# Kernel tuning notes

Hardware: AMD Instinct MI355X
Metric: run time of the kernel (lower is better)

Reference implementation:

```python
import jax, jax.numpy as jnp
import numpy as np

N, D, R, E = 10000, 1024, 8, 80000


def setup_inputs() -> dict:
    key = jax.random.key(0)
    ks = jax.random.split(key, 8)
    s = 1.0 / np.sqrt(D)
    x = jax.random.normal(ks[0], (N, D), dtype=jnp.float32)
    edge_index = jax.random.randint(ks[1], (2, E), 0, N, dtype=jnp.int64)
    edge_type = jax.random.randint(ks[2], (E,), 0, R, dtype=jnp.int64)
    weight = jax.random.normal(ks[3], (R, D, D), dtype=jnp.float32) * s  # per-relation W_r
    root = jax.random.normal(ks[4], (D, D), dtype=jnp.float32) * s      # root/self-loop weight
    bias = jnp.zeros((D,), dtype=jnp.float32)
    w_gate = jax.random.normal(ks[5], (2 * D, D), dtype=jnp.float32) * (1.0 / np.sqrt(2 * D))
    b_gate = jnp.zeros((D,), dtype=jnp.float32)
    return {"x": x, "edge_index": edge_index, "edge_type": edge_type,
            "weight": weight, "root": root, "bias": bias,
            "w_gate": w_gate, "b_gate": b_gate}


def _rgcn(x, edge_index, edge_type, weight, root, bias):
    # PyG RGCNConv (aggr='mean'): per relation r, mean-aggregate x[src] into dst,
    # then transform by W_r (aggregate-then-transform, equivalent by linearity).
    src, dst = edge_index[0], edge_index[1]
    msgs = x[src]                                   # [E, D] gather
    out = x @ root + bias                           # root/self connection
    n = x.shape[0]
    for r in range(weight.shape[0]):                # small fixed relation loop
        mask = (edge_type == r).astype(x.dtype)     # [E]
        sums = jax.ops.segment_sum(msgs * mask[:, None], dst, num_segments=n)
        cnt = jax.ops.segment_sum(mask, dst, num_segments=n)
        mean = sums / jnp.maximum(cnt, 1.0)[:, None]
        out = out + mean @ weight[r]
    return out


def reference(x, edge_index, edge_type, weight, root, bias, w_gate, b_gate):
    u = _rgcn(x, edge_index, edge_type, weight, root, bias)
    # dropout p=0 -> identity
    z = jnp.concatenate([u, x], axis=1) @ w_gate + b_gate
    h = jnp.tanh(u) * z + x * (1.0 - z)
    return h
```

## Files before the change

kernel.cpp:

```cpp
#include <hip/hip_runtime.h>
#include <math.h>

typedef unsigned short u16;
typedef __attribute__((ext_vector_type(8))) short bf16x8;
typedef __attribute__((ext_vector_type(4))) float f32x4;

static constexpr int kN = 10000;
static constexpr int kNpad = 10240;
static constexpr int kD = 1024;
static constexpr int kR = 8;
static constexpr int kE = 80000;
static constexpr int kKz = 2 * kD;
static constexpr int kCrows = kNpad * (kR + 1);
static constexpr int kTilesY1 = kCrows / 128;

#define GLB(p) ((const __attribute__((address_space(1))) unsigned int*)(const void*)(p))
#define LDSP(p) ((__attribute__((address_space(3))) unsigned int*)(p))

__device__ __forceinline__ u16 f2bf(float f) {
    union { float f; unsigned int i; } c; c.f = f;
    unsigned int u = c.i;
    return (u16)((u + 0x7FFFu + ((u >> 16) & 1u)) >> 16);
}
__device__ __forceinline__ float bf2f(u16 u) {
    union { unsigned int i; float f; } c; c.i = ((unsigned int)u) << 16;
    return c.f;
}
__device__ __forceinline__ ushort4 f2bf4(float4 v) {
    ushort4 o; o.x = f2bf(v.x); o.y = f2bf(v.y); o.z = f2bf(v.z); o.w = f2bf(v.w);
    return o;
}

__global__ void zero16(uint4* __restrict__ p, long n16) {
    long i = (long)blockIdx.x * blockDim.x + threadIdx.x;
    long st = (long)gridDim.x * blockDim.x;
    uint4 z = make_uint4(0, 0, 0, 0);
    for (; i < n16; i += st) p[i] = z;
}

__global__ void mark_edges(const int* __restrict__ src, const int* __restrict__ dst,
                           const int* __restrict__ etype,
                           int* __restrict__ cntd, int* __restrict__ flag) {
    int e = blockIdx.x * blockDim.x + threadIdx.x;
    if (e < kE) {
        atomicAdd(&cntd[dst[e]], 1);
        flag[etype[e] * kN + src[e]] = 1;
    }
}

__global__ __launch_bounds__(1024) void scan_rowptr(const int* __restrict__ cnt,
                                                    int* __restrict__ rowptr,
                                                    int* __restrict__ cursor) {
    __shared__ int wsum[16];
    __shared__ int carry;
    const int tid = threadIdx.x;
    const int lane = tid & 63;
    const int w = tid >> 6;
    if (tid == 0) carry = 0;
    const int nchunk = (kN + 1024) / 1024;
    for (int ch = 0; ch < nchunk; ++ch) {
        int idx = ch * 1024 + tid;
        int v = (idx < kN) ? cnt[idx] : 0;
        int s = v;
#pragma unroll
        for (int off = 1; off < 64; off <<= 1) {
            int t = __shfl_up(s, off, 64);
            if (lane >= off) s += t;
        }
        if (lane == 63) wsum[w] = s;
        __syncthreads();
        if (w == 0 && lane < 16) {
            int t = wsum[lane];
#pragma unroll
            for (int off = 1; off < 16; off <<= 1) {
                int tt = __shfl_up(t, off, 64);
                if (lane >= off) t += tt;
            }
            wsum[lane] = t;
        }
        __syncthreads();
        int wpre = (w > 0) ? wsum[w - 1] : 0;
        int incl = s + wpre + carry;
        int excl = incl - v;
        if (idx <= kN) rowptr[idx] = excl;
        if (idx < kN) cursor[idx] = 0;
        __syncthreads();
        if (tid == 1023) carry = incl;
        __syncthreads();
    }
}

__global__ __launch_bounds__(1024) void compact_scan(const int* __restrict__ flag,
                                                     int* __restrict__ row_src,
                                                     int* __restrict__ pos_tab,
                                                     int* __restrict__ relcnt9) {
    const int tid = threadIdx.x;
    if (blockIdx.x == kR) {
        for (int i = tid; i < kNpad; i += 1024) row_src[i] = i;
        if (tid == 0) relcnt9[0] = kN;
        return;
    }
    const int r = blockIdx.x;
    const int base = kNpad * (r + 1);
    __shared__ int wsum[16];
    __shared__ int carry;
    const int lane = tid & 63;
    const int w = tid >> 6;
    if (tid == 0) carry = 0;
    const int nchunk = (kN + 1023) / 1024;
    for (int ch = 0; ch < nchunk; ++ch) {
        int idx = ch * 1024 + tid;
        int v = (idx < kN) ? flag[r * kN + idx] : 0;
        int s = v;
#pragma unroll
        for (int off = 1; off < 64; off <<= 1) {
            int t = __shfl_up(s, off, 64);
            if (lane >= off) s += t;
        }
        if (lane == 63) wsum[w] = s;
        __syncthreads();
        if (w == 0 && lane < 16) {
            int t = wsum[lane];
#pragma unroll
            for (int off = 1; off < 16; off <<= 1) {
                int tt = __shfl_up(t, off, 64);
                if (lane >= off) t += tt;
            }
            wsum[lane] = t;
        }
        __syncthreads();
        int wpre = (w > 0) ? wsum[w - 1] : 0;
        int incl = s + wpre + carry;
        int excl = incl - v;
        if (idx < kN && v) {
            row_src[base + excl] = idx;
            pos_tab[r * kN + idx] = base + excl;
        }
        __syncthreads();
        if (tid == 1023) carry = incl;
        __syncthreads();
    }
    if (tid == 0) relcnt9[r + 1] = carry;
}

__global__ void fill_edges(const int* __restrict__ src, const int* __restrict__ dst,
                           const int* __restrict__ etype, const int* __restrict__ rowptr,
                           int* __restrict__ cursor, const int* __restrict__ pos_tab,
                           int* __restrict__ erec) {
    int e = blockIdx.x * blockDim.x + threadIdx.x;
    if (e < kE) {
        int d = dst[e], r = etype[e], s = src[e];
        int pos = rowptr[d] + atomicAdd(&cursor[d], 1);
        erec[pos] = (pos_tab[r * kN + s] << 3) | r;
    }
}

__global__ void cvt_x(const float* __restrict__ x, u16* __restrict__ ga) {
    int row = blockIdx.x;
    int c = threadIdx.x << 2;
    float4 v = *reinterpret_cast<const float4*>(x + (size_t)row * kD + c);
    *reinterpret_cast<ushort4*>(ga + (size_t)row * kKz + kD + c) = f2bf4(v);
}

__global__ void transpose_to_bf16(const float* __restrict__ S, u16* __restrict__ D,
                                  int rows, int cols, int ldD) {
    S += (size_t)blockIdx.z * rows * cols;
    D += (size_t)blockIdx.z * rows * cols;
    __shared__ float t[32][33];
    int c0 = blockIdx.x * 32, r0 = blockIdx.y * 32;
    int x = threadIdx.x, y = threadIdx.y;
#pragma unroll
    for (int i = 0; i < 32; i += 8)
        t[y + i][x] = S[(size_t)(r0 + y + i) * cols + c0 + x];
    __syncthreads();
#pragma unroll
    for (int i = 0; i < 32; i += 8)
        D[(size_t)(c0 + y + i) * ldD + r0 + x] = f2bf(t[x][y + i]);
}

__global__ __launch_bounds__(256) void aggregate(const u16* __restrict__ yc,
                                                 const float* __restrict__ bias,
                                                 const int* __restrict__ rowptr,
                                                 const int* __restrict__ erec,
                                                 u16* __restrict__ ga) {
    const int d = blockIdx.x;
    const int c = threadIdx.x << 2;
    const int e0 = rowptr[d], e1 = rowptr[d + 1];

    __shared__ float rs[kR];
    if (threadIdx.x == 0) {
        int cc[kR] = {0, 0, 0, 0, 0, 0, 0, 0};
        for (int e = e0; e < e1; ++e) cc[erec[e] & 7]++;
#pragma unroll
        for (int r = 0; r < kR; ++r) rs[r] = 1.0f / fmaxf((float)cc[r], 1.0f);
    }
    __syncthreads();

    ushort4 rv = *reinterpret_cast<const ushort4*>(yc + (size_t)d * kD + c);
    float4 bv = *reinterpret_cast<const float4*>(bias + c);
    float4 acc = make_float4(bf2f(rv.x) + bv.x, bf2f(rv.y) + bv.y,
                             bf2f(rv.z) + bv.z, bf2f(rv.w) + bv.w);

    int e = e0;
    for (; e + 3 < e1; e += 4) {
        int rec0 = erec[e], rec1 = erec[e + 1], rec2 = erec[e + 2], rec3 = erec[e + 3];
        ushort4 v0 = *reinterpret_cast<const ushort4*>(yc + (size_t)(rec0 >> 3) * kD + c);
        ushort4 v1 = *reinterpret_cast<const ushort4*>(yc + (size_t)(rec1 >> 3) * kD + c);
        ushort4 v2 = *reinterpret_cast<const ushort4*>(yc + (size_t)(rec2 >> 3) * kD + c);
        ushort4 v3 = *reinterpret_cast<const ushort4*>(yc + (size_t)(rec3 >> 3) * kD + c);
        float s0 = rs[rec0 & 7], s1 = rs[rec1 & 7], s2 = rs[rec2 & 7], s3 = rs[rec3 & 7];
        acc.x += s0 * bf2f(v0.x); acc.y += s0 * bf2f(v0.y);
        acc.z += s0 * bf2f(v0.z); acc.w += s0 * bf2f(v0.w);
        acc.x += s1 * bf2f(v1.x); acc.y += s1 * bf2f(v1.y);
        acc.z += s1 * bf2f(v1.z); acc.w += s1 * bf2f(v1.w);
        acc.x += s2 * bf2f(v2.x); acc.y += s2 * bf2f(v2.y);
        acc.z += s2 * bf2f(v2.z); acc.w += s2 * bf2f(v2.w);
        acc.x += s3 * bf2f(v3.x); acc.y += s3 * bf2f(v3.y);
        acc.z += s3 * bf2f(v3.z); acc.w += s3 * bf2f(v3.w);
    }
    for (; e < e1; ++e) {
        int rec = erec[e];
        float sc = rs[rec & 7];
        ushort4 v = *reinterpret_cast<const ushort4*>(yc + (size_t)(rec >> 3) * kD + c);
        acc.x += sc * bf2f(v.x); acc.y += sc * bf2f(v.y);
        acc.z += sc * bf2f(v.z); acc.w += sc * bf2f(v.w);
    }
    *reinterpret_cast<ushort4*>(ga + (size_t)d * kKz + c) = f2bf4(acc);
}

__global__ __launch_bounds__(256, 3) void gemm_compact(
    const u16* __restrict__ xb, int ldx,
    const u16* __restrict__ Bt9,
    const int* __restrict__ row_src, const int* __restrict__ relcnt9,
    u16* __restrict__ yc)
{
    const int t0 = blockIdx.y;
    const int relidx = t0 / 80;
    const int lt = t0 - relidx * 80;
    if (lt * 128 >= relcnt9[relidx]) return;

    __shared__ u16 sA[3][128 * 32];
    __shared__ u16 sB[3][128 * 32];

    const int tid = threadIdx.x;
    const int wave = tid >> 6;
    const int lane = tid & 63;

    const int row0 = t0 * 128;
    const int col0 = blockIdx.x * 128;

    const int srow = wave * 16 + (lane >> 2);
    const int scol = (((lane & 3) ^ ((srow >> 1) & 3)) * 8);

    const u16* gA0 = xb + (size_t)row_src[row0 + srow] * ldx + scol;
    const u16* gA1 = xb + (size_t)row_src[row0 + 64 + srow] * ldx + scol;
    const u16* gB0 = Bt9 + (size_t)(relidx * kD + col0 + srow) * kD + scol;
    const u16* gB1 = Bt9 + (size_t)(relidx * kD + col0 + 64 + srow) * kD + scol;

    const int lof0 = (wave * 16) * 32;
    const int lof1 = (64 + wave * 16) * 32;

    const int mq = (wave >> 1) * 64;
    const int nq = (wave & 1) * 64;
    const int fm = lane & 15;
    const int fkx = (((lane >> 4) ^ ((fm >> 1) & 3))) * 8;

    f32x4 zf = {0.0f, 0.0f, 0.0f, 0.0f};
    f32x4 acc[4][4];
#pragma unroll
    for (int i = 0; i < 4; ++i)
#pragma unroll
        for (int j = 0; j < 4; ++j) acc[i][j] = zf;

    auto stage = [&](int s) {
        __builtin_amdgcn_global_load_lds(GLB(gA0), LDSP(sA[s] + lof0), 16, 0, 0);
        __builtin_amdgcn_global_load_lds(GLB(gA1), LDSP(sA[s] + lof1), 16, 0, 0);
        __builtin_amdgcn_global_load_lds(GLB(gB0), LDSP(sB[s] + lof0), 16, 0, 0);
        __builtin_amdgcn_global_load_lds(GLB(gB1), LDSP(sB[s] + lof1), 16, 0, 0);
        gA0 += 32; gA1 += 32; gB0 += 32; gB1 += 32;
    };

    constexpr int T = kD / 32;
    stage(0);
    stage(1);

    int s = 0;
    for (int t = 0; t < T; ++t) {
        if (t + 2 < T) {
            stage(s == 0 ? 2 : (s - 1));
            asm volatile("s_waitcnt vmcnt(8)" ::: "memory");
        } else if (t + 1 < T) {
            asm volatile("s_waitcnt vmcnt(4)" ::: "memory");
        } else {
            asm volatile("s_waitcnt vmcnt(0)" ::: "memory");
        }
        __builtin_amdgcn_s_barrier();
        asm volatile("" ::: "memory");

        const u16* cA = sA[s];
        const u16* cB = sB[s];
        bf16x8 af[4], bfr[4];
#pragma unroll
        for (int i = 0; i < 4; ++i)
            af[i] = *reinterpret_cast<const bf16x8*>(&cA[(mq + i * 16 + fm) * 32 + fkx]);
#pragma unroll
        for (int j = 0; j < 4; ++j)
            bfr[j] = *reinterpret_cast<const bf16x8*>(&cB[(nq + j * 16 + fm) * 32 + fkx]);
#pragma unroll
        for (int i = 0; i < 4; ++i)
#pragma unroll
            for (int j = 0; j < 4; ++j)
                acc[i][j] = __builtin_amdgcn_mfma_f32_16x16x32_bf16(bfr[j], af[i], acc[i][j], 0, 0, 0);

        asm volatile("" ::: "memory");
        __builtin_amdgcn_s_barrier();
        s = (s == 2) ? 0 : (s + 1);
    }

    const int cq = (lane >> 4) * 4;
#pragma unroll
    for (int i = 0; i < 4; ++i) {
        int row = row0 + mq + i * 16 + fm;
#pragma unroll
        for (int j = 0; j < 4; ++j) {
            int col = col0 + nq + j * 16 + cq;
            f32x4 v = acc[i][j];
            ushort4 o;
            o.x = f2bf(v[0]); o.y = f2bf(v[1]); o.z = f2bf(v[2]); o.w = f2bf(v[3]);
            *reinterpret_cast<ushort4*>(yc + (size_t)row * kD + col) = o;
        }
    }
}

__global__ __launch_bounds__(256, 3) void gemm_mfma_gate(
    const u16* __restrict__ A, int lda,
    const u16* __restrict__ Bt, int ldb, int K,
    int M, const float* __restrict__ bias,
    float* __restrict__ Cf, const u16* __restrict__ uga, const float* __restrict__ xo)
{
    __shared__ u16 sA[3][128 * 32];
    __shared__ u16 sB[3][128 * 32];

    const int tid = threadIdx.x;
    const int wave = tid >> 6;
    const int lane = tid & 63;

    constexpr int GX = kD / 128;
    constexpr int GY = kNpad / 128;
    const int lin = blockIdx.y * GX + blockIdx.x;
    const int xcd = lin & 7;
    const int pos = lin >> 3;
    const int ty = xcd * (GY / 8) + (pos >> 3);
    const int tx = pos & 7;

    const int row0 = ty * 128;
    const int col0 = tx * 128;

    const int srow = wave * 16 + (lane >> 2);
    const int scol = (((lane & 3) ^ ((srow >> 1) & 3)) * 8);

    const u16* gA0 = A + (size_t)(row0 + srow) * lda + scol;
    const u16* gA1 = A + (size_t)(row0 + 64 + srow) * lda + scol;
    const u16* gB0 = Bt + (size_t)(col0 + srow) * ldb + scol;
    const u16* gB1 = Bt + (size_t)(col0 + 64 + srow) * ldb + scol;

    const int lof0 = (wave * 16) * 32;
    const int lof1 = (64 + wave * 16) * 32;

    const int mq = (wave >> 1) * 64;
    const int nq = (wave & 1) * 64;
    const int fm = lane & 15;
    const int fkx = (((lane >> 4) ^ ((fm >> 1) & 3))) * 8;

    f32x4 zf = {0.0f, 0.0f, 0.0f, 0.0f};
    f32x4 acc[4][4];
#pragma unroll
    for (int i = 0; i < 4; ++i)
#pragma unroll
        for (int j = 0; j < 4; ++j) acc[i][j] = zf;

    auto stage = [&](int s) {
        __builtin_amdgcn_global_load_lds(GLB(gA0), LDSP(sA[s] + lof0), 16, 0, 0);
        __builtin_amdgcn_global_load_lds(GLB(gA1), LDSP(sA[s] + lof1), 16, 0, 0);
        __builtin_amdgcn_global_load_lds(GLB(gB0), LDSP(sB[s] + lof0), 16, 0, 0);
        __builtin_amdgcn_global_load_lds(GLB(gB1), LDSP(sB[s] + lof1), 16, 0, 0);
        gA0 += 32; gA1 += 32; gB0 += 32; gB1 += 32;
    };

    const int T = K >> 5;
    stage(0);
    stage(1);

    int s = 0;
    for (int t = 0; t < T; ++t) {
        if (t + 2 < T) {
            stage(s == 0 ? 2 : (s - 1));
            asm volatile("s_waitcnt vmcnt(8)" ::: "memory");
        } else if (t + 1 < T) {
            asm volatile("s_waitcnt vmcnt(4)" ::: "memory");
        } else {
            asm volatile("s_waitcnt vmcnt(0)" ::: "memory");
        }
        __builtin_amdgcn_s_barrier();
        asm volatile("" ::: "memory");

        const u16* cA = sA[s];
        const u16* cB = sB[s];
        bf16x8 af[4], bfr[4];
#pragma unroll
        for (int i = 0; i < 4; ++i)
            af[i] = *reinterpret_cast<const bf16x8*>(&cA[(mq + i * 16 + fm) * 32 + fkx]);
#pragma unroll
        for (int j = 0; j < 4; ++j)
            bfr[j] = *reinterpret_cast<const bf16x8*>(&cB[(nq + j * 16 + fm) * 32 + fkx]);
#pragma unroll
        for (int i = 0; i < 4; ++i)
#pragma unroll
            for (int j = 0; j < 4; ++j)
                acc[i][j] = __builtin_amdgcn_mfma_f32_16x16x32_bf16(bfr[j], af[i], acc[i][j], 0, 0, 0);

        asm volatile("" ::: "memory");
        __builtin_amdgcn_s_barrier();
        s = (s == 2) ? 0 : (s + 1);
    }

    const int cq = (lane >> 4) * 4;
#pragma unroll
    for (int i = 0; i < 4; ++i) {
        int row = row0 + mq + i * 16 + fm;
        if (row >= M) continue;
#pragma unroll
        for (int j = 0; j < 4; ++j) {
            int col = col0 + nq + j * 16 + cq;
            f32x4 v = acc[i][j];
            float4 bv = *reinterpret_cast<const float4*>(bias + col);
            v[0] += bv.x; v[1] += bv.y; v[2] += bv.z; v[3] += bv.w;
            ushort4 ur = *reinterpret_cast<const ushort4*>(uga + (size_t)row * kKz + col);
            float4 xr = *reinterpret_cast<const float4*>(xo + (size_t)row * kD + col);
            float4 h;
            h.x = tanhf(bf2f(ur.x)) * v[0] + xr.x * (1.0f - v[0]);
            h.y = tanhf(bf2f(ur.y)) * v[1] + xr.y * (1.0f - v[1]);
            h.z = tanhf(bf2f(ur.z)) * v[2] + xr.z * (1.0f - v[2]);
            h.w = tanhf(bf2f(ur.w)) * v[3] + xr.w * (1.0f - v[3]);
            *reinterpret_cast<float4*>(Cf + (size_t)row * kD + col) = h;
        }
    }
}

extern "C" void kernel_launch(void* const* d_in, const int* in_sizes, int n_in,
                              void* d_out, int out_size, void* d_ws, size_t ws_size,
                              hipStream_t stream) {
    (void)in_sizes; (void)n_in; (void)out_size; (void)ws_size;

    const float* x     = (const float*)d_in[0];
    const int* eidx    = (const int*)d_in[1];
    const int* etype   = (const int*)d_in[2];
    const float* weight= (const float*)d_in[3];
    const float* root  = (const float*)d_in[4];
    const float* bias  = (const float*)d_in[5];
    const float* wgate = (const float*)d_in[6];
    const float* bgate = (const float*)d_in[7];
    float* out = (float*)d_out;

    const int* src = eidx;
    const int* dst = eidx + kE;

    char* ws = (char*)d_ws;
    size_t off = 0;
    u16* yc   = (u16*)(ws + off);    off += (size_t)kCrows * kD * 2;
    u16* ga   = (u16*)(ws + off);    off += (size_t)kNpad * kKz * 2;
    u16* Bt9  = (u16*)(ws + off);    off += (size_t)(kR + 1) * kD * kD * 2;
    u16* wg_t = (u16*)(ws + off);    off += (size_t)kD * kKz * 2;
    int* cntd    = (int*)(ws + off); off += (size_t)kN * 4;
    int* flag    = (int*)(ws + off); off += (size_t)kR * kN * 4;
    int* row_src = (int*)(ws + off); off += (size_t)kCrows * 4;
    int* pos_tab = (int*)(ws + off); off += (size_t)kR * kN * 4;
    int* rowp    = (int*)(ws + off); off += (size_t)(kN + 16) * 4;
    int* curs    = (int*)(ws + off); off += (size_t)kN * 4;
    int* erec    = (int*)(ws + off); off += (size_t)kE * 4;
    int* relcnt9 = (int*)(ws + off); off += 16 * 4;

    zero16<<<180, 256, 0, stream>>>((uint4*)cntd, (long)(kN + kR * kN + kCrows) / 4);

    mark_edges<<<(kE + 255) / 256, 256, 0, stream>>>(src, dst, etype, cntd, flag);
    scan_rowptr<<<1, 1024, 0, stream>>>(cntd, rowp, curs);
    compact_scan<<<kR + 1, 1024, 0, stream>>>(flag, row_src, pos_tab, relcnt9);
    fill_edges<<<(kE + 255) / 256, 256, 0, stream>>>(src, dst, etype, rowp, curs,
                                                     pos_tab, erec);

    zero16<<<256, 256, 0, stream>>>((uint4*)(ga + (size_t)kN * kKz),
                                    (long)(kNpad - kN) * kKz * 2 / 16);

    cvt_x<<<kN, 256, 0, stream>>>(x, ga);

    {
        dim3 b(32, 8);
        transpose_to_bf16<<<dim3(kD / 32, kD / 32, 1), b, 0, stream>>>(root, Bt9, kD, kD, kD);
        transpose_to_bf16<<<dim3(kD / 32, kD / 32, kR), b, 0, stream>>>(
            weight, Bt9 + (size_t)kD * kD, kD, kD, kD);
        transpose_to_bf16<<<dim3(kD / 32, kKz / 32, 1), b, 0, stream>>>(wgate, wg_t, kKz, kD, kKz);
    }

    dim3 g1(kD / 128, kTilesY1);
    gemm_compact<<<g1, 256, 0, stream>>>(ga + kD, kKz, Bt9, row_src, relcnt9, yc);

    aggregate<<<kN, 256, 0, stream>>>(yc, bias, rowp, erec, ga);

    dim3 g2(kD / 128, kNpad / 128);
    gemm_mfma_gate<<<g2, 256, 0, stream>>>(ga, kKz, wg_t, kKz, kKz, kN, bgate, out, ga, x);
}
```

Measured before the change: 475.9 us.

## Enlarge compacted GEMM tiles to 256x256 with 512 threads and BK=64 double buffering

The per-relation compacted GEMM moves from 128x128 tiles with 256 threads and a 3-stage BK=32 pipeline to 256x256 tiles with 8 waves, BK=64 and a 2-stage buffer. Each wave now computes a 128x64 sub-tile, the LDS swizzle changes to an 8-way XOR, and s_setprio is raised around the MFMA bursts. The aim is more operand reuse per global load and fewer barriers per K step. The cost is more accumulator registers, 128KB of LDS per block, and coarser tail handling, since a partially filled relation tile now wastes up to 255 rows.

```diff
diff --git a/kernel.cpp b/kernel.cpp
--- a/kernel.cpp
+++ b/kernel.cpp
@@ -12,7 +12,6 @@
 static constexpr int kE = 80000;
 static constexpr int kKz = 2 * kD;
 static constexpr int kCrows = kNpad * (kR + 1);
-static constexpr int kTilesY1 = kCrows / 128;
 
 #define GLB(p) ((const __attribute__((address_space(1))) unsigned int*)(const void*)(p))
 #define LDSP(p) ((__attribute__((address_space(3))) unsigned int*)(p))
@@ -228,102 +227,122 @@
     *reinterpret_cast<ushort4*>(ga + (size_t)d * kKz + c) = f2bf4(acc);
 }
 
-__global__ __launch_bounds__(256, 3) void gemm_compact(
+__global__ __launch_bounds__(512, 2) void gemm_compact(
     const u16* __restrict__ xb, int ldx,
     const u16* __restrict__ Bt9,
     const int* __restrict__ row_src, const int* __restrict__ relcnt9,
     u16* __restrict__ yc)
 {
     const int t0 = blockIdx.y;
-    const int relidx = t0 / 80;
-    const int lt = t0 - relidx * 80;
-    if (lt * 128 >= relcnt9[relidx]) return;
-
-    __shared__ u16 sA[3][128 * 32];
-    __shared__ u16 sB[3][128 * 32];
+    const int relidx = t0 / 40;
+    const int lt = t0 - relidx * 40;
+    if (lt * 256 >= relcnt9[relidx]) return;
+
+    __shared__ u16 sA[2][256 * 64];
+    __shared__ u16 sB[2][256 * 64];
 
     const int tid = threadIdx.x;
     const int wave = tid >> 6;
     const int lane = tid & 63;
 
-    const int row0 = t0 * 128;
-    const int col0 = blockIdx.x * 128;
-
-    const int srow = wave * 16 + (lane >> 2);
-    const int scol = (((lane & 3) ^ ((srow >> 1) & 3)) * 8);
-
-    const u16* gA0 = xb + (size_t)row_src[row0 + srow] * ldx + scol;
-    const u16* gA1 = xb + (size_t)row_src[row0 + 64 + srow] * ldx + scol;
-    const u16* gB0 = Bt9 + (size_t)(relidx * kD + col0 + srow) * kD + scol;
-    const u16* gB1 = Bt9 + (size_t)(relidx * kD + col0 + 64 + srow) * kD + scol;
-
-    const int lof0 = (wave * 16) * 32;
-    const int lof1 = (64 + wave * 16) * 32;
-
-    const int mq = (wave >> 1) * 64;
-    const int nq = (wave & 1) * 64;
+    const int row0 = t0 * 256;
+    const int col0 = blockIdx.x * 256;
+
+    const int s_row = tid >> 3;
+    const int s_src = ((tid & 7) ^ (s_row & 7)) * 8;
+    const int wbase = wave * 512;
+
+    const u16* gA[4];
+    const u16* gB[4];
+#pragma unroll
+    for (int q = 0; q < 4; ++q) {
+        gA[q] = xb + (size_t)row_src[row0 + q * 64 + s_row] * ldx + s_src;
+        gB[q] = Bt9 + (size_t)(relidx * kD + col0 + q * 64 + s_row) * kD + s_src;
+    }
+
+    auto stage = [&](int b) {
+        u16* dA = &sA[b][0];
+        u16* dB = &sB[b][0];
+#pragma unroll
+        for (int q = 0; q < 4; ++q) {
+            __builtin_amdgcn_global_load_lds(GLB(gA[q]), LDSP(dA + q * 4096 + wbase), 16, 0, 0);
+            gA[q] += 64;
+        }
+#pragma unroll
+        for (int q = 0; q < 4; ++q) {
+            __builtin_amdgcn_global_load_lds(GLB(gB[q]), LDSP(dB + q * 4096 + wbase), 16, 0, 0);
+            gB[q] += 64;
+        }
+    };
+
+    const int wm = (wave >> 2) * 128;
+    const int wn = (wave & 3) * 64;
     const int fm = lane & 15;
-    const int fkx = (((lane >> 4) ^ ((fm >> 1) & 3))) * 8;
+    const int g4 = lane >> 4;
+    const int pc0 = ((g4) ^ (fm & 7)) * 8;
+    const int pc1 = ((4 | g4) ^ (fm & 7)) * 8;
 
     f32x4 zf = {0.0f, 0.0f, 0.0f, 0.0f};
-    f32x4 acc[4][4];
-#pragma unroll
-    for (int i = 0; i < 4; ++i)
+    f32x4 acc[8][4];
+#pragma unroll
+    for (int i = 0; i < 8; ++i)
 #pragma unroll
         for (int j = 0; j < 4; ++j) acc[i][j] = zf;
 
-    auto stage = [&](int s) {
-        __builtin_amdgcn_global_load_lds(GLB(gA0), LDSP(sA[s] + lof0), 16, 0, 0);
-        __builtin_amdgcn_global_load_lds(GLB(gA1), LDSP(sA[s] + lof1), 16, 0, 0);
-        __builtin_amdgcn_global_load_lds(GLB(gB0), LDSP(sB[s] + lof0), 16, 0, 0);
-        __builtin_amdgcn_global_load_lds(GLB(gB1), LDSP(sB[s] + lof1), 16, 0, 0);
-        gA0 += 32; gA1 += 32; gB0 += 32; gB1 += 32;
-    };
-
-    constexpr int T = kD / 32;
+    constexpr int T = kD / 64;
     stage(0);
     stage(1);
 
-    int s = 0;
     for (int t = 0; t < T; ++t) {
-        if (t + 2 < T) {
-            stage(s == 0 ? 2 : (s - 1));
-            asm volatile("s_waitcnt vmcnt(8)" ::: "memory");
-        } else if (t + 1 < T) {
-            asm volatile("s_waitcnt vmcnt(4)" ::: "memory");
-        } else {
-            asm volatile("s_waitcnt vmcnt(0)" ::: "memory");
-        }
+        if (t + 1 < T) asm volatile("s_waitcnt vmcnt(8)" ::: "memory");
+        else           asm volatile("s_waitcnt vmcnt(0)" ::: "memory");
         __builtin_amdgcn_s_barrier();
         asm volatile("" ::: "memory");
 
-        const u16* cA = sA[s];
-        const u16* cB = sB[s];
-        bf16x8 af[4], bfr[4];
-#pragma unroll
-        for (int i = 0; i < 4; ++i)
-            af[i] = *reinterpret_cast<const bf16x8*>(&cA[(mq + i * 16 + fm) * 32 + fkx]);
+        const u16* cA = sA[t & 1];
+        const u16* cB = sB[t & 1];
+        bf16x8 af[8], bfv[4];
+
+#pragma unroll
+        for (int i = 0; i < 8; ++i)
+            af[i] = *reinterpret_cast<const bf16x8*>(&cA[(wm + i * 16 + fm) * 64 + pc0]);
 #pragma unroll
         for (int j = 0; j < 4; ++j)
-            bfr[j] = *reinterpret_cast<const bf16x8*>(&cB[(nq + j * 16 + fm) * 32 + fkx]);
-#pragma unroll
-        for (int i = 0; i < 4; ++i)
+            bfv[j] = *reinterpret_cast<const bf16x8*>(&cB[(wn + j * 16 + fm) * 64 + pc0]);
+        __builtin_amdgcn_s_setprio(1);
+#pragma unroll
+        for (int i = 0; i < 8; ++i)
 #pragma unroll
             for (int j = 0; j < 4; ++j)
-                acc[i][j] = __builtin_amdgcn_mfma_f32_16x16x32_bf16(bfr[j], af[i], acc[i][j], 0, 0, 0);
+                acc[i][j] = __builtin_amdgcn_mfma_f32_16x16x32_bf16(bfv[j], af[i], acc[i][j], 0, 0, 0);
+        __builtin_amdgcn_s_setprio(0);
+
+#pragma unroll
+        for (int i = 0; i < 8; ++i)
+            af[i] = *reinterpret_cast<const bf16x8*>(&cA[(wm + i * 16 + fm) * 64 + pc1]);
+#pragma unroll
+        for (int j = 0; j < 4; ++j)
+            bfv[j] = *reinterpret_cast<const bf16x8*>(&cB[(wn + j * 16 + fm) * 64 + pc1]);
+        __builtin_amdgcn_s_setprio(1);
+#pragma unroll
+        for (int i = 0; i < 8; ++i)
+#pragma unroll
+            for (int j = 0; j < 4; ++j)
+                acc[i][j] = __builtin_amdgcn_mfma_f32_16x16x32_bf16(bfv[j], af[i], acc[i][j], 0, 0, 0);
+        __builtin_amdgcn_s_setprio(0);
 
         asm volatile("" ::: "memory");
         __builtin_amdgcn_s_barrier();
-        s = (s == 2) ? 0 : (s + 1);
-    }
-
-    const int cq = (lane >> 4) * 4;
-#pragma unroll
-    for (int i = 0; i < 4; ++i) {
-        int row = row0 + mq + i * 16 + fm;
+        if (t + 2 < T) stage(t & 1);
+    }
+
+    const int cq = g4 * 4;
+#pragma unroll
+    for (int i = 0; i < 8; ++i) {
+        int row = row0 + wm + i * 16 + fm;
 #pragma unroll
         for (int j = 0; j < 4; ++j) {
-            int col = col0 + nq + j * 16 + cq;
+            int col = col0 + wn + j * 16 + cq;
             f32x4 v = acc[i][j];
             ushort4 o;
             o.x = f2bf(v[0]); o.y = f2bf(v[1]); o.z = f2bf(v[2]); o.w = f2bf(v[3]);
@@ -501,8 +520,8 @@
         transpose_to_bf16<<<dim3(kD / 32, kKz / 32, 1), b, 0, stream>>>(wgate, wg_t, kKz, kD, kKz);
     }
 
-    dim3 g1(kD / 128, kTilesY1);
-    gemm_compact<<<g1, 256, 0, stream>>>(ga + kD, kKz, Bt9, row_src, relcnt9, yc);
+    dim3 g1(kD / 256, kCrows / 256);
+    gemm_compact<<<g1, 512, 0, stream>>>(ga + kD, kKz, Bt9, row_src, relcnt9, yc);
 
     aggregate<<<kN, 256, 0, stream>>>(yc, bias, rowp, erec, ga);
 
```

Result: no change. 478.0 us (+0.5%).
